# Kernel tuning notes

Measured on AMD Instinct MI355X. Metric: run time of the kernel, lower is better.

## Reference

```python
import jax, jax.numpy as jnp
import numpy as np

N = 50000   # nodes
E = 800000  # edges
F = 64      # input features
H = 64      # hidden (nhid)
C = 10      # classes
G = 500     # graphs in batch


def setup_inputs() -> dict:
    key = jax.random.key(0)
    ks = jax.random.split(key, 12)
    s = lambda fan: np.float32(1.0 / np.sqrt(fan))
    return {
        "x": jax.random.normal(ks[0], (N, F), jnp.float32),
        "edge_index": jax.random.randint(ks[1], (2, E), 0, N, dtype=jnp.int64),
        "batch": jnp.sort(jax.random.randint(ks[2], (N,), 0, G, dtype=jnp.int64)),
        "W1": jax.random.normal(ks[3], (F, H), jnp.float32) * s(F),
        "b1": jnp.zeros((H,), jnp.float32),
        "W2": jax.random.normal(ks[4], (H, H), jnp.float32) * s(H),
        "b2": jnp.zeros((H,), jnp.float32),
        "W3": jax.random.normal(ks[5], (H, H), jnp.float32) * s(H),
        "b3": jnp.zeros((H,), jnp.float32),
        "lin1_W": jax.random.normal(ks[6], (H, H), jnp.float32) * s(H),
        "lin1_b": jnp.zeros((H,), jnp.float32),
        "lin2_W": jax.random.normal(ks[7], (H, C), jnp.float32) * s(H),
        "lin2_b": jnp.zeros((C,), jnp.float32),
    }


def reference(x, edge_index, batch, W1, b1, W2, b2, W3, b3, lin1_W, lin1_b, lin2_W, lin2_b):
    n = x.shape[0]
    loops = jnp.arange(n, dtype=edge_index.dtype)
    src = jnp.concatenate([edge_index[0], loops])  # message sources (x_j)
    dst = jnp.concatenate([edge_index[1], loops])  # aggregation targets
    # symmetric GCN normalization on A + I
    deg = jax.ops.segment_sum(jnp.ones(src.shape, x.dtype), dst, num_segments=n)
    dis = jax.lax.rsqrt(deg)  # deg >= 1 thanks to self-loops
    norm = (dis[src] * dis[dst])[:, None]  # [E+N, 1]

    def gcn_relu(h, W, b):
        h = h @ W                                   # [N, H]
        agg = jax.ops.segment_sum(h[src] * norm, dst, num_segments=n)
        return jax.nn.relu(agg + b)

    h = gcn_relu(x, W1, b1)
    h = gcn_relu(h, W2, b2)
    h = gcn_relu(h, W3, b3)

    # global mean pool per graph
    sums = jax.ops.segment_sum(h, batch, num_segments=G)
    counts = jax.ops.segment_sum(jnp.ones((n,), h.dtype), batch, num_segments=G)
    pooled = sums / jnp.maximum(counts, 1.0)[:, None]  # [G, H]

    h = jax.nn.relu(pooled @ lin1_W + lin1_b)
    # dropout is identity in eval mode
    logits = h @ lin2_W + lin2_b
    return jax.nn.log_softmax(logits, axis=-1)
```

## Files before the change

### kernel.cpp

```cpp
#include <hip/hip_runtime.h>

#define NN 50000
#define NE 800000
#define HD 64
#define NC 10
#define NG 500
#define CAP 64
#define NBLK 196
#define NPART 8
#define PSZ 6250
#define FILLB 2048
#define MBLK 782

typedef float f32x4 __attribute__((ext_vector_type(4)));
typedef short bf16x8 __attribute__((ext_vector_type(8)));

__device__ __forceinline__ float bf16_to_f32(unsigned short h) {
    union { unsigned int u; float f; } v;
    v.u = ((unsigned int)h) << 16;
    return v.f;
}
__device__ __forceinline__ unsigned short f32_to_bf16(float f) {
    union { float f; unsigned int u; } v;
    v.f = f;
    unsigned int r = v.u + 0x7FFFu + ((v.u >> 16) & 1u);
    return (unsigned short)(r >> 16);
}

__device__ __forceinline__ float gather_relu(
    const unsigned short* __restrict__ tin, int wid, int colv, int c0,
    float di, float bv, int lane) {
    int cnt = c0 > CAP ? CAP : c0;
    float acc[8];
#pragma unroll
    for (int j = 0; j < 8; ++j) acc[j] = 0.f;
    acc[0] = bf16_to_f32(tin[(size_t)wid * HD + lane]);
    int e = 0;
    for (; e + 7 < cnt; e += 8) {
#pragma unroll
        for (int j = 0; j < 8; ++j) {
            int s = __shfl(colv, e + j);
            acc[j] += bf16_to_f32(tin[(size_t)s * HD + lane]);
        }
    }
    for (; e < cnt; ++e) {
        int s = __shfl(colv, e);
        acc[0] += bf16_to_f32(tin[(size_t)s * HD + lane]);
    }
    float s01 = (acc[0] + acc[1]) + (acc[2] + acc[3]);
    float s23 = (acc[4] + acc[5]) + (acc[6] + acc[7]);
    return fmaxf((s01 + s23) * di + bv, 0.f);
}

__device__ __forceinline__ void load_wfrags(const float* __restrict__ W, int lane,
                                            bf16x8 bh[4][2], bf16x8 bl[4][2]) {
    int col = lane & 15, krow = (lane >> 4) * 8;
#pragma unroll
    for (int n = 0; n < 4; ++n)
#pragma unroll
        for (int kt = 0; kt < 2; ++kt)
#pragma unroll
            for (int j = 0; j < 8; ++j) {
                float wv = W[(kt * 32 + krow + j) * 64 + n * 16 + col];
                unsigned short h = f32_to_bf16(wv);
                float rem = wv - bf16_to_f32(h);
                bh[n][kt][j] = (short)h;
                bl[n][kt][j] = (short)f32_to_bf16(rem);
            }
}

__global__ void init_k(int* __restrict__ rowcnt, float* __restrict__ pooled) {
    int i = blockIdx.x * 256 + threadIdx.x;
    if (i < NN) rowcnt[i] = 0;
    if (i < NG * HD) pooled[i] = 0.f;
}

__global__ __launch_bounds__(256) void fill3_k(
    const int* __restrict__ src, const int* __restrict__ dst,
    int* __restrict__ rowcnt, unsigned short* __restrict__ col16) {
    int part = blockIdx.x & (NPART - 1);
    int blk = blockIdx.x >> 3;
    int dlo = part * PSZ, dhi = dlo + PSZ;
    int stride = (FILLB / NPART) * 256;
    for (int e = blk * 256 + threadIdx.x; e < NE; e += stride) {
        int d = dst[e];
        if (d >= dlo && d < dhi) {
            int p = atomicAdd(&rowcnt[d], 1);
            if (p < CAP) col16[(size_t)d * CAP + p] = (unsigned short)src[e];
        }
    }
}

__global__ __launch_bounds__(256) void mfma_gemm1_k(
    const float* __restrict__ x, const float* __restrict__ W,
    const int* __restrict__ rowcnt, unsigned short* __restrict__ out16) {
    __shared__ unsigned short A[64][72];
    int t = threadIdx.x, lane = t & 63, w = t >> 6;
    int base = blockIdx.x * 64;
#pragma unroll
    for (int i = 0; i < 4; ++i) {
        int idx = t + i * 256;
        int row = idx >> 4, c4 = (idx & 15) * 4;
        int r = base + row;
        float4 v = make_float4(0.f, 0.f, 0.f, 0.f);
        if (r < NN) v = ((const float4*)x)[(size_t)r * 16 + (idx & 15)];
        unsigned int p0 = f32_to_bf16(v.x) | ((unsigned int)f32_to_bf16(v.y) << 16);
        unsigned int p1 = f32_to_bf16(v.z) | ((unsigned int)f32_to_bf16(v.w) << 16);
        *(unsigned int*)&A[row][c4] = p0;
        *(unsigned int*)&A[row][c4 + 2] = p1;
    }
    bf16x8 bh[4][2], bl[4][2];
    load_wfrags(W, lane, bh, bl);
    __syncthreads();
    int col = lane & 15, krow = (lane >> 4) * 8;
    bf16x8 a0 = *(const bf16x8*)&A[w * 16 + col][krow];
    bf16x8 a1 = *(const bf16x8*)&A[w * 16 + col][32 + krow];
    f32x4 acc[4];
#pragma unroll
    for (int n = 0; n < 4; ++n) { acc[n] = (f32x4){0.f, 0.f, 0.f, 0.f}; }
#pragma unroll
    for (int n = 0; n < 4; ++n) {
        acc[n] = __builtin_amdgcn_mfma_f32_16x16x32_bf16(a0, bh[n][0], acc[n], 0, 0, 0);
        acc[n] = __builtin_amdgcn_mfma_f32_16x16x32_bf16(a1, bh[n][1], acc[n], 0, 0, 0);
        acc[n] = __builtin_amdgcn_mfma_f32_16x16x32_bf16(a0, bl[n][0], acc[n], 0, 0, 0);
        acc[n] = __builtin_amdgcn_mfma_f32_16x16x32_bf16(a1, bl[n][1], acc[n], 0, 0, 0);
    }
    int row0 = base + w * 16 + (lane >> 4) * 4;
    float di[4];
#pragma unroll
    for (int r = 0; r < 4; ++r)
        di[r] = (row0 + r < NN) ? rsqrtf((float)(rowcnt[row0 + r] + 1)) : 1.f;
#pragma unroll
    for (int n = 0; n < 4; ++n)
#pragma unroll
        for (int r = 0; r < 4; ++r) {
            int row = row0 + r;
            if (row < NN)
                out16[(size_t)row * HD + n * 16 + col] = f32_to_bf16(acc[n][r] * di[r]);
        }
}

__global__ __launch_bounds__(512) void agg_mfma_k(
    const unsigned short* __restrict__ tin, const int* __restrict__ rowcnt,
    const unsigned short* __restrict__ col16, const float* __restrict__ bias,
    const float* __restrict__ W, unsigned short* __restrict__ tout) {
    __shared__ unsigned short A[64][72];
    __shared__ unsigned short Whi[64][72];
    __shared__ unsigned short Wlo[64][72];
    __shared__ float dibuf[64];
    int t = threadIdx.x, lane = t & 63, w = t >> 6;
    int base = blockIdx.x * 64;
    float bv = bias[lane];
    int colv[8], c0[8];
#pragma unroll
    for (int n = 0; n < 8; ++n) {
        int wid = base + w * 8 + n;
        bool v = wid < NN;
        colv[n] = v ? (int)col16[(size_t)wid * CAP + lane] : 0;
        c0[n] = v ? rowcnt[wid] : -1;
    }
#pragma unroll
    for (int i = 0; i < 8; ++i) {
        int idx = t + i * 512;
        int k = idx >> 6, c = idx & 63;
        float wv = W[idx];
        unsigned short h = f32_to_bf16(wv);
        Whi[c][k] = h;
        Wlo[c][k] = f32_to_bf16(wv - bf16_to_f32(h));
    }
#pragma unroll
    for (int n = 0; n < 8; ++n) {
        int row = w * 8 + n;
        float r = 0.f, di = 1.f;
        if (c0[n] >= 0) {
            di = rsqrtf((float)(c0[n] + 1));
            r = gather_relu(tin, base + row, colv[n], c0[n], di, bv, lane);
        }
        A[row][lane] = f32_to_bf16(r);
        if (lane == 0) dibuf[row] = di;
    }
    __syncthreads();
    if (w >= 4) return;
    int col = lane & 15, krow = (lane >> 4) * 8;
    bf16x8 a0 = *(const bf16x8*)&A[w * 16 + col][krow];
    bf16x8 a1 = *(const bf16x8*)&A[w * 16 + col][32 + krow];
    float dr[4];
#pragma unroll
    for (int r = 0; r < 4; ++r) dr[r] = dibuf[w * 16 + (lane >> 4) * 4 + r];
    int row0 = base + w * 16 + (lane >> 4) * 4;
#pragma unroll
    for (int n = 0; n < 4; ++n) {
        bf16x8 bh0 = *(const bf16x8*)&Whi[n * 16 + col][krow];
        bf16x8 bh1 = *(const bf16x8*)&Whi[n * 16 + col][32 + krow];
        bf16x8 bl0 = *(const bf16x8*)&Wlo[n * 16 + col][krow];
        bf16x8 bl1 = *(const bf16x8*)&Wlo[n * 16 + col][32 + krow];
        f32x4 acc = (f32x4){0.f, 0.f, 0.f, 0.f};
        acc = __builtin_amdgcn_mfma_f32_16x16x32_bf16(a0, bh0, acc, 0, 0, 0);
        acc = __builtin_amdgcn_mfma_f32_16x16x32_bf16(a1, bh1, acc, 0, 0, 0);
        acc = __builtin_amdgcn_mfma_f32_16x16x32_bf16(a0, bl0, acc, 0, 0, 0);
        acc = __builtin_amdgcn_mfma_f32_16x16x32_bf16(a1, bl1, acc, 0, 0, 0);
#pragma unroll
        for (int r = 0; r < 4; ++r) {
            int row = row0 + r;
            if (row < NN)
                tout[(size_t)row * HD + n * 16 + col] = f32_to_bf16(acc[r] * dr[r]);
        }
    }
}

__global__ __launch_bounds__(512) void agg_pool_k(
    const unsigned short* __restrict__ tin, const int* __restrict__ rowcnt,
    const unsigned short* __restrict__ col16, const float* __restrict__ bias,
    const int* __restrict__ batch, float* __restrict__ pooled) {
    int t = threadIdx.x, lane = t & 63, w = t >> 6;
    int base = blockIdx.x * 64 + w * 8;
    float bv = bias[lane];
    int colv[8], c0[8];
#pragma unroll
    for (int n = 0; n < 8; ++n) {
        int wid = base + n;
        bool v = wid < NN;
        colv[n] = v ? (int)col16[(size_t)wid * CAP + lane] : 0;
        c0[n] = v ? rowcnt[wid] : -1;
    }
    int curg = -1;
    float psum = 0.f;
#pragma unroll
    for (int n = 0; n < 8; ++n) {
        if (c0[n] >= 0) {
            int wid = base + n;
            float di = rsqrtf((float)(c0[n] + 1));
            float r = gather_relu(tin, wid, colv[n], c0[n], di, bv, lane);
            int g = batch[wid];
            if (g != curg) {
                if (curg >= 0) atomicAdd(&pooled[(size_t)curg * HD + lane], psum);
                curg = g;
                psum = r;
            } else {
                psum += r;
            }
        }
    }
    if (curg >= 0) atomicAdd(&pooled[(size_t)curg * HD + lane], psum);
}

__global__ __launch_bounds__(64) void poolhead_k(
    const float* __restrict__ pooled, const int* __restrict__ batch,
    const float* __restrict__ l1W, const float* __restrict__ l1b,
    const float* __restrict__ l2W, const float* __restrict__ l2b,
    float* __restrict__ out) {
    __shared__ float p[64];
    __shared__ float hsm[64];
    __shared__ float lg[NC];
    __shared__ int ss[2];
    int g = blockIdx.x, t = threadIdx.x;
    if (t < 2) {
        int target = g + t;
        int lo = 0, hi = NN;
        while (lo < hi) {
            int mid = (lo + hi) >> 1;
            if (batch[mid] < target) lo = mid + 1; else hi = mid;
        }
        ss[t] = lo;
    }
    __syncthreads();
    float c = (float)(ss[1] - ss[0]);
    p[t] = pooled[(size_t)g * HD + t] / fmaxf(c, 1.0f);
    __syncthreads();
    float a = l1b[t];
#pragma unroll
    for (int k = 0; k < 64; ++k) a += p[k] * l1W[k * 64 + t];
    hsm[t] = fmaxf(a, 0.f);
    __syncthreads();
    if (t < NC) {
        float a2 = l2b[t];
#pragma unroll
        for (int k = 0; k < 64; ++k) a2 += hsm[k] * l2W[k * NC + t];
        lg[t] = a2;
    }
    __syncthreads();
    if (t < NC) {
        float m = -1e30f;
#pragma unroll
        for (int k = 0; k < NC; ++k) m = fmaxf(m, lg[k]);
        float s = 0.f;
#pragma unroll
        for (int k = 0; k < NC; ++k) s += expf(lg[k] - m);
        out[(size_t)g * NC + t] = lg[t] - m - logf(s);
    }
}

extern "C" void kernel_launch(void* const* d_in, const int* in_sizes, int n_in,
                              void* d_out, int out_size, void* d_ws, size_t ws_size,
                              hipStream_t stream) {
    const float* x = (const float*)d_in[0];
    const int* ei = (const int*)d_in[1];
    const int* src = ei;
    const int* dst = ei + NE;
    const int* batch = (const int*)d_in[2];
    const float* W1 = (const float*)d_in[3];
    const float* b1 = (const float*)d_in[4];
    const float* W2 = (const float*)d_in[5];
    const float* b2 = (const float*)d_in[6];
    const float* W3 = (const float*)d_in[7];
    const float* b3 = (const float*)d_in[8];
    const float* l1W = (const float*)d_in[9];
    const float* l1b = (const float*)d_in[10];
    const float* l2W = (const float*)d_in[11];
    const float* l2b = (const float*)d_in[12];
    float* out = (float*)d_out;

    char* p = (char*)d_ws;
    auto alloc = [&](size_t bytes) {
        char* r = p;
        p += (bytes + 255) & ~(size_t)255;
        return r;
    };
    int* rowcnt = (int*)alloc(NN * 4);
    unsigned short* col16 = (unsigned short*)alloc((size_t)NN * CAP * 2);
    unsigned short* tmpA = (unsigned short*)alloc((size_t)NN * HD * 2);
    unsigned short* tmpB = (unsigned short*)alloc((size_t)NN * HD * 2);
    float* pooled = (float*)alloc((size_t)NG * HD * 4);

    init_k<<<NBLK, 256, 0, stream>>>(rowcnt, pooled);
    fill3_k<<<FILLB, 256, 0, stream>>>(src, dst, rowcnt, col16);

    mfma_gemm1_k<<<MBLK, 256, 0, stream>>>(x, W1, rowcnt, tmpA);
    agg_mfma_k<<<MBLK, 512, 0, stream>>>(tmpA, rowcnt, col16, b1, W2, tmpB);
    agg_mfma_k<<<MBLK, 512, 0, stream>>>(tmpB, rowcnt, col16, b2, W3, tmpA);
    agg_pool_k<<<MBLK, 512, 0, stream>>>(tmpA, rowcnt, col16, b3, batch, pooled);

    poolhead_k<<<NG, 64, 0, stream>>>(pooled, batch, l1W, l1b, l2W, l2b, out);
}
```

Before: 244.4 us.

## Split adjacency into 32-slot main rows plus overflow array, pack two rows per wavefront

The padded neighbour list is split into a dense 32-entry array and a separate overflow array for nodes with more than 32 in-edges. Each wavefront now loads two nodes' 32-entry lists with one 64-lane load and reads the 8 row counts with a single load plus shuffles. With an average in-degree of about 16, this halves the bytes read for column indices and cuts the number of load instructions. The cost is an extra branch and a scattered overflow read for high-degree nodes, plus slightly more complex indexing.

```diff
diff --git a/kernel.cpp b/kernel.cpp
--- a/kernel.cpp
+++ b/kernel.cpp
@@ -6,6 +6,7 @@
 #define NC 10
 #define NG 500
 #define CAP 64
+#define CAPR 32
 #define NBLK 196
 #define NPART 8
 #define PSZ 6250
@@ -28,24 +29,32 @@
 }
 
 __device__ __forceinline__ float gather_relu(
-    const unsigned short* __restrict__ tin, int wid, int colv, int c0,
-    float di, float bv, int lane) {
+    const unsigned short* __restrict__ tin, const unsigned short* __restrict__ ovf,
+    int wid, int colv, int sel, int c0, float di, float bv, int lane) {
     int cnt = c0 > CAP ? CAP : c0;
+    int cmain = cnt > CAPR ? CAPR : cnt;
     float acc[8];
 #pragma unroll
     for (int j = 0; j < 8; ++j) acc[j] = 0.f;
     acc[0] = bf16_to_f32(tin[(size_t)wid * HD + lane]);
     int e = 0;
-    for (; e + 7 < cnt; e += 8) {
+    for (; e + 7 < cmain; e += 8) {
 #pragma unroll
         for (int j = 0; j < 8; ++j) {
-            int s = __shfl(colv, e + j);
+            int s = __shfl(colv, sel + e + j);
             acc[j] += bf16_to_f32(tin[(size_t)s * HD + lane]);
         }
     }
-    for (; e < cnt; ++e) {
-        int s = __shfl(colv, e);
+    for (; e < cmain; ++e) {
+        int s = __shfl(colv, sel + e);
         acc[0] += bf16_to_f32(tin[(size_t)s * HD + lane]);
+    }
+    if (cnt > CAPR) {
+        int co = ovf[(size_t)wid * CAPR + (lane & 31)];
+        for (int e2 = CAPR; e2 < cnt; ++e2) {
+            int s = __shfl(co, e2 - CAPR);
+            acc[0] += bf16_to_f32(tin[(size_t)s * HD + lane]);
+        }
     }
     float s01 = (acc[0] + acc[1]) + (acc[2] + acc[3]);
     float s23 = (acc[4] + acc[5]) + (acc[6] + acc[7]);
@@ -77,7 +86,8 @@
 
 __global__ __launch_bounds__(256) void fill3_k(
     const int* __restrict__ src, const int* __restrict__ dst,
-    int* __restrict__ rowcnt, unsigned short* __restrict__ col16) {
+    int* __restrict__ rowcnt, unsigned short* __restrict__ col32,
+    unsigned short* __restrict__ ovf) {
     int part = blockIdx.x & (NPART - 1);
     int blk = blockIdx.x >> 3;
     int dlo = part * PSZ, dhi = dlo + PSZ;
@@ -86,7 +96,8 @@
         int d = dst[e];
         if (d >= dlo && d < dhi) {
             int p = atomicAdd(&rowcnt[d], 1);
-            if (p < CAP) col16[(size_t)d * CAP + p] = (unsigned short)src[e];
+            if (p < CAPR) col32[(size_t)d * CAPR + p] = (unsigned short)src[e];
+            else if (p < CAP) ovf[(size_t)d * CAPR + (p - CAPR)] = (unsigned short)src[e];
         }
     }
 }
@@ -142,8 +153,9 @@
 
 __global__ __launch_bounds__(512) void agg_mfma_k(
     const unsigned short* __restrict__ tin, const int* __restrict__ rowcnt,
-    const unsigned short* __restrict__ col16, const float* __restrict__ bias,
-    const float* __restrict__ W, unsigned short* __restrict__ tout) {
+    const unsigned short* __restrict__ col32, const unsigned short* __restrict__ ovf,
+    const float* __restrict__ bias, const float* __restrict__ W,
+    unsigned short* __restrict__ tout) {
     __shared__ unsigned short A[64][72];
     __shared__ unsigned short Whi[64][72];
     __shared__ unsigned short Wlo[64][72];
@@ -151,13 +163,20 @@
     int t = threadIdx.x, lane = t & 63, w = t >> 6;
     int base = blockIdx.x * 64;
     float bv = bias[lane];
-    int colv[8], c0[8];
+    int cidx = base + w * 8 + (lane & 7);
+    int cnt8 = rowcnt[cidx < NN ? cidx : NN - 1];
+    int colv2[4];
+#pragma unroll
+    for (int np = 0; np < 4; ++np) {
+        int wid2 = base + w * 8 + np * 2 + (lane >= 32 ? 1 : 0);
+        if (wid2 >= NN) wid2 = NN - 1;
+        colv2[np] = col32[(size_t)wid2 * CAPR + (lane & 31)];
+    }
+    int c0[8];
 #pragma unroll
     for (int n = 0; n < 8; ++n) {
-        int wid = base + w * 8 + n;
-        bool v = wid < NN;
-        colv[n] = v ? (int)col16[(size_t)wid * CAP + lane] : 0;
-        c0[n] = v ? rowcnt[wid] : -1;
+        int v = __shfl(cnt8, n);
+        c0[n] = (base + w * 8 + n < NN) ? v : -1;
     }
 #pragma unroll
     for (int i = 0; i < 8; ++i) {
@@ -174,7 +193,8 @@
         float r = 0.f, di = 1.f;
         if (c0[n] >= 0) {
             di = rsqrtf((float)(c0[n] + 1));
-            r = gather_relu(tin, base + row, colv[n], c0[n], di, bv, lane);
+            r = gather_relu(tin, ovf, base + row, colv2[n >> 1], (n & 1) * 32,
+                            c0[n], di, bv, lane);
         }
         A[row][lane] = f32_to_bf16(r);
         if (lane == 0) dibuf[row] = di;
@@ -210,18 +230,26 @@
 
 __global__ __launch_bounds__(512) void agg_pool_k(
     const unsigned short* __restrict__ tin, const int* __restrict__ rowcnt,
-    const unsigned short* __restrict__ col16, const float* __restrict__ bias,
-    const int* __restrict__ batch, float* __restrict__ pooled) {
+    const unsigned short* __restrict__ col32, const unsigned short* __restrict__ ovf,
+    const float* __restrict__ bias, const int* __restrict__ batch,
+    float* __restrict__ pooled) {
     int t = threadIdx.x, lane = t & 63, w = t >> 6;
     int base = blockIdx.x * 64 + w * 8;
     float bv = bias[lane];
-    int colv[8], c0[8];
+    int cidx = base + (lane & 7);
+    int cnt8 = rowcnt[cidx < NN ? cidx : NN - 1];
+    int colv2[4];
+#pragma unroll
+    for (int np = 0; np < 4; ++np) {
+        int wid2 = base + np * 2 + (lane >= 32 ? 1 : 0);
+        if (wid2 >= NN) wid2 = NN - 1;
+        colv2[np] = col32[(size_t)wid2 * CAPR + (lane & 31)];
+    }
+    int c0[8];
 #pragma unroll
     for (int n = 0; n < 8; ++n) {
-        int wid = base + n;
-        bool v = wid < NN;
-        colv[n] = v ? (int)col16[(size_t)wid * CAP + lane] : 0;
-        c0[n] = v ? rowcnt[wid] : -1;
+        int v = __shfl(cnt8, n);
+        c0[n] = (base + n < NN) ? v : -1;
     }
     int curg = -1;
     float psum = 0.f;
@@ -230,7 +258,8 @@
         if (c0[n] >= 0) {
             int wid = base + n;
             float di = rsqrtf((float)(c0[n] + 1));
-            float r = gather_relu(tin, wid, colv[n], c0[n], di, bv, lane);
+            float r = gather_relu(tin, ovf, wid, colv2[n >> 1], (n & 1) * 32,
+                                  c0[n], di, bv, lane);
             int g = batch[wid];
             if (g != curg) {
                 if (curg >= 0) atomicAdd(&pooled[(size_t)curg * HD + lane], psum);
@@ -317,18 +346,19 @@
         return r;
     };
     int* rowcnt = (int*)alloc(NN * 4);
-    unsigned short* col16 = (unsigned short*)alloc((size_t)NN * CAP * 2);
+    unsigned short* col32 = (unsigned short*)alloc((size_t)NN * CAPR * 2);
+    unsigned short* ovf = (unsigned short*)alloc((size_t)NN * CAPR * 2);
     unsigned short* tmpA = (unsigned short*)alloc((size_t)NN * HD * 2);
     unsigned short* tmpB = (unsigned short*)alloc((size_t)NN * HD * 2);
     float* pooled = (float*)alloc((size_t)NG * HD * 4);
 
     init_k<<<NBLK, 256, 0, stream>>>(rowcnt, pooled);
-    fill3_k<<<FILLB, 256, 0, stream>>>(src, dst, rowcnt, col16);
+    fill3_k<<<FILLB, 256, 0, stream>>>(src, dst, rowcnt, col32, ovf);
 
     mfma_gemm1_k<<<MBLK, 256, 0, stream>>>(x, W1, rowcnt, tmpA);
-    agg_mfma_k<<<MBLK, 512, 0, stream>>>(tmpA, rowcnt, col16, b1, W2, tmpB);
-    agg_mfma_k<<<MBLK, 512, 0, stream>>>(tmpB, rowcnt, col16, b2, W3, tmpA);
-    agg_pool_k<<<MBLK, 512, 0, stream>>>(tmpA, rowcnt, col16, b3, batch, pooled);
+    agg_mfma_k<<<MBLK, 512, 0, stream>>>(tmpA, rowcnt, col32, ovf, b1, W2, tmpB);
+    agg_mfma_k<<<MBLK, 512, 0, stream>>>(tmpB, rowcnt, col32, ovf, b2, W3, tmpA);
+    agg_pool_k<<<MBLK, 512, 0, stream>>>(tmpA, rowcnt, col32, ovf, b3, batch, pooled);
 
     poolhead_k<<<NG, 64, 0, stream>>>(pooled, batch, l1W, l1b, l2W, l2b, out);
 }
```

Result: faster. 229.8 us (median of 2 runs) (-6.0%).
